# Kernel tuning notes

Measured on AMD Instinct MI355X. Metric: run time of the kernel, lower is better.

## Reference

```python
import jax, jax.numpy as jnp
import numpy as np

B, T, D, H = 8, 2048, 512, 128

def setup_inputs() -> dict:
    key = jax.random.key(0)
    ks = jax.random.split(key, 8)
    s = lambda fan_in: 1.0 / np.sqrt(fan_in)
    return {
        "x": jax.random.normal(ks[0], (B, T, D), jnp.float32),
        "prediction": jax.random.normal(ks[1], (B, T, D), jnp.float32),
        "Wq": jax.random.uniform(ks[2], (D, H), jnp.float32, -s(D), s(D)),
        "bq": jnp.zeros((H,), jnp.float32),
        "Wk": jax.random.uniform(ks[3], (D, H), jnp.float32, -s(D), s(D)),
        "bk": jnp.zeros((H,), jnp.float32),
        "Wv": jax.random.uniform(ks[4], (D, D), jnp.float32, -s(D), s(D)),
        "bv": jnp.zeros((D,), jnp.float32),
        "Wf": jax.random.uniform(ks[5], (2 * D, D), jnp.float32, -s(2 * D), s(2 * D)),
        "bf": jnp.zeros((D,), jnp.float32),
    }

def reference(x, prediction, Wq, bq, Wk, bk, Wv, bv, Wf, bf):
    # q,k: [B,T,H]; v: [B,T,D]
    q = jnp.einsum('btd,dh->bth', prediction, Wq) + bq
    k = jnp.einsum('btd,dh->bth', x, Wk) + bk
    v = jnp.einsum('btd,de->bte', x, Wv) + bv
    # unscaled attention scores [B,T,T]
    scores = jnp.einsum('bth,bsh->bts', q, k)
    attn = jax.nn.softmax(scores, axis=-1)
    attended = jnp.einsum('bts,bsd->btd', attn, v)
    fusion_input = jnp.concatenate([prediction, attended], axis=-1)  # [B,T,2D]
    return jax.nn.sigmoid(jnp.einsum('btf,fd->btd', fusion_input, Wf) + bf)
```

## Files before the change

### kernel.cpp

```cpp
#include <hip/hip_runtime.h>
#include <hip/hip_bf16.h>


#define APF_B 8
#define APF_T 2048
#define APF_D 512
#define APF_H 128
#define APF_M (APF_B * APF_T)

typedef unsigned short u16;
typedef __attribute__((ext_vector_type(8))) short short8;
typedef __attribute__((ext_vector_type(4))) float f32x4;

static __device__ __forceinline__ float bf2f(u16 u) {
    union { unsigned int i; float f; } w;
    w.i = ((unsigned int)u) << 16;
    return w.f;
}
static __device__ __forceinline__ u16 f2bf(float x) {
    union { float f; unsigned int u; } cv;
    cv.f = x;
    unsigned int u = cv.u + 0x7FFFu + ((cv.u >> 16) & 1u);
    return (u16)(u >> 16);
}

static __device__ __forceinline__ void load16_lds(const u16* g, u16* l) {
    __builtin_amdgcn_global_load_lds(
        (const __attribute__((address_space(1))) unsigned int*)g,
        (__attribute__((address_space(3))) unsigned int*)l,
        16, 0, 0);
}


__global__ __launch_bounds__(256) void cvt_pair(const float* __restrict__ in0,
                                                u16* __restrict__ out0,
                                                const float* __restrict__ in1,
                                                u16* __restrict__ out1, long n4)
{
    long i = blockIdx.x * 256L + threadIdx.x;
    const long stride = (long)gridDim.x * 256L;
    for (; i < 2 * n4; i += stride) {
        const float* in = (i < n4) ? in0 : in1;
        u16* out = (i < n4) ? out0 : out1;
        const long j = (i < n4) ? i : (i - n4);
        const float4 v = ((const float4*)in)[j];
        ushort4 o;
        o.x = f2bf(v.x); o.y = f2bf(v.y); o.z = f2bf(v.z); o.w = f2bf(v.w);
        ((ushort4*)out)[j] = o;
    }
}

__global__ __launch_bounds__(256) void prep_weights(
    const float* __restrict__ Wq, u16* __restrict__ WqT,
    const float* __restrict__ Wk, u16* __restrict__ WkT,
    const float* __restrict__ Wv, u16* __restrict__ WvT,
    const float* __restrict__ Wf, u16* __restrict__ WfT)
{
    const long e = blockIdx.x * 256L + threadIdx.x;
    if (e < 65536) {
        const long idx = e;
        const long n = idx / 512, k = idx % 512;
        WqT[idx] = f2bf(Wq[k * 128 + n]);
    } else if (e < 131072) {
        const long idx = e - 65536;
        const long n = idx / 512, k = idx % 512;
        WkT[idx] = f2bf(Wk[k * 128 + n]);
    } else if (e < 393216) {
        const long idx = e - 131072;
        const long n = idx / 512, k = idx % 512;
        WvT[idx] = f2bf(Wv[k * 512 + n]);
    } else if (e < 917504) {
        const long idx = e - 393216;
        const long n = idx / 1024, k = idx % 1024;
        WfT[idx] = f2bf(Wf[k * 512 + n]);
    }
}

template <int DUAL, int EPI>
__global__ __launch_bounds__(256) void mfma_gemm(
    const u16* __restrict__ Ap, const u16* __restrict__ A2p, long lda,
    const u16* __restrict__ Bp, const u16* __restrict__ Bp2, long ldb,
    const float* __restrict__ biasp, const float* __restrict__ bias2,
    void* __restrict__ Cp, void* __restrict__ Cp2, long ldc, int K,
    long sA, long sB, long sC)
{
    __shared__ u16 smA[128 * 32];
    __shared__ u16 smB[128 * 32];

    const int tid  = threadIdx.x;
    const int lane = tid & 63;
    const int wid  = tid >> 6;
    const int wr   = wid >> 1;
    const int wc   = wid & 1;

    const long row0 = (long)blockIdx.y * 128;
    const long col0 = (long)blockIdx.x * 128;
    const long z    = blockIdx.z;

    const u16* Abase = (DUAL == 2) ? (z ? A2p : Ap) : (Ap + z * sA);
    const u16* Bbase = (DUAL == 2) ? (z ? Bp2 : Bp) : (Bp + z * sB);

    f32x4 acc[4][4];
#pragma unroll
    for (int i = 0; i < 4; ++i)
#pragma unroll
        for (int j = 0; j < 4; ++j)
            acc[i][j] = (f32x4){0.f, 0.f, 0.f, 0.f};

    const int lrow = (lane >> 4) * 4;
    const int lcol = lane & 15;
    const int q8   = (lane >> 4) * 8;

    for (int kb = 0; kb < K; kb += 32) {
#pragma unroll
        for (int rep = 0; rep < 2; ++rep) {
            const int c  = tid + rep * 256;
            const int r  = c >> 2;
            const int kc = (c & 3) * 8;
            const int wbase = (wid * 64 + rep * 256) * 8;
            const u16* ga;
            if (DUAL == 1 && (kb + kc) >= APF_D) {
                ga = A2p + (row0 + r) * lda + (kb + kc - APF_D);
            } else {
                ga = Abase + (row0 + r) * lda + (kb + kc);
            }
            load16_lds(ga, &smA[wbase]);
            const u16* gb = Bbase + (col0 + r) * ldb + (kb + kc);
            load16_lds(gb, &smB[wbase]);
        }
        __syncthreads();

        short8 av[4], bv4[4];
#pragma unroll
        for (int ti = 0; ti < 4; ++ti)
            av[ti] = *(const short8*)&smA[(wr * 64 + ti * 16 + lcol) * 32 + q8];
#pragma unroll
        for (int tj = 0; tj < 4; ++tj)
            bv4[tj] = *(const short8*)&smB[(wc * 64 + tj * 16 + lcol) * 32 + q8];

#pragma unroll
        for (int ti = 0; ti < 4; ++ti)
#pragma unroll
            for (int tj = 0; tj < 4; ++tj)
                acc[ti][tj] = __builtin_amdgcn_mfma_f32_16x16x32_bf16(
                    av[ti], bv4[tj], acc[ti][tj], 0, 0, 0);
        __syncthreads();
    }

    const float* bias = (DUAL == 2 && z) ? bias2 : biasp;

#pragma unroll
    for (int ti = 0; ti < 4; ++ti) {
        const long m0t = row0 + wr * 64 + ti * 16 + lrow;
#pragma unroll
        for (int tj = 0; tj < 4; ++tj) {
            const long n = col0 + wc * 64 + tj * 16 + lcol;
            const float bn = (bias != nullptr) ? bias[n] : 0.f;
            if (EPI == 0) {
                u16* C = (u16*)((DUAL == 2 && z) ? Cp2 : Cp) + ((DUAL == 2) ? 0 : z * sC);
#pragma unroll
                for (int r = 0; r < 4; ++r)
                    C[(m0t + r) * ldc + n] = f2bf(acc[ti][tj][r] + bn);
            } else if (EPI == 1) {
                u16* C = (u16*)Cp;
                const long b  = m0t >> 11;
                const long ml = m0t & 2047;
                ushort4 pk;
                pk.x = f2bf(acc[ti][tj][0] + bn);
                pk.y = f2bf(acc[ti][tj][1] + bn);
                pk.z = f2bf(acc[ti][tj][2] + bn);
                pk.w = f2bf(acc[ti][tj][3] + bn);
                *(ushort4*)&C[b * (512L * 2048) + n * 2048 + ml] = pk;
            } else {
                float* C = (float*)Cp;
#pragma unroll
                for (int r = 0; r < 4; ++r) {
                    const float val = acc[ti][tj][r] + bn;
                    C[(m0t + r) * ldc + n] = 1.0f / (1.0f + expf(-val));
                }
            }
        }
    }
}

#define FA_LDQ 136
#define FA_LDK 136
#define FA_LDV 72
#define FA_LDP 72

__global__ __launch_bounds__(512, 2) void attn_fused(
    const u16* __restrict__ qg, const u16* __restrict__ kg,
    const u16* __restrict__ vTg, u16* __restrict__ attg)
{
    __shared__ u16 sQ[128 * FA_LDQ];
    __shared__ u16 sK[64 * FA_LDK];
    __shared__ u16 sV[256 * FA_LDV];
    __shared__ u16 sP[128 * FA_LDP];

    const int tid  = threadIdx.x;
    const int lane = tid & 63;
    const int w    = tid >> 6;
    const int l15  = lane & 15;
    const int q4   = lane >> 4;

    const long z  = blockIdx.z;
    const long q0 = (long)blockIdx.y * 128;
    const long d0 = (long)blockIdx.x * 256;

    {
        const u16* src = qg + (z * APF_T + q0) * APF_H;
#pragma unroll
        for (int rep = 0; rep < 4; ++rep) {
            const int c   = tid + rep * 512;
            const int row = c >> 4;
            const int c8  = (c & 15) * 8;
            *(uint4*)&sQ[row * FA_LDQ + c8] = *(const uint4*)(src + (long)c * 8);
        }
    }

    f32x4 oacc[16];
#pragma unroll
    for (int i = 0; i < 16; ++i) oacc[i] = (f32x4){0.f, 0.f, 0.f, 0.f};
    float rs[4] = {0.f, 0.f, 0.f, 0.f};

    for (int kt = 0; kt < APF_T / 64; ++kt) {
        __syncthreads();
        {
            const u16* src = kg + (z * APF_T + (long)kt * 64) * APF_H;
#pragma unroll
            for (int rep = 0; rep < 2; ++rep) {
                const int c   = tid + rep * 512;
                const int row = c >> 4;
                const int c8  = (c & 15) * 8;
                *(uint4*)&sK[row * FA_LDK + c8] = *(const uint4*)(src + (long)c * 8);
            }
        }
        {
            const u16* src = vTg + z * ((long)APF_D * APF_T) + d0 * APF_T + (long)kt * 64;
#pragma unroll
            for (int rep = 0; rep < 4; ++rep) {
                const int c   = tid + rep * 512;
                const int row = c >> 3;
                const int c8  = (c & 7) * 8;
                *(uint4*)&sV[row * FA_LDV + c8] =
                    *(const uint4*)(src + (long)row * APF_T + c8);
            }
        }
        __syncthreads();

        f32x4 sacc[4];
#pragma unroll
        for (int tj = 0; tj < 4; ++tj) sacc[tj] = (f32x4){0.f, 0.f, 0.f, 0.f};
#pragma unroll
        for (int kk = 0; kk < 4; ++kk) {
            const short8 av = *(const short8*)&sQ[(w * 16 + l15) * FA_LDQ + kk * 32 + q4 * 8];
#pragma unroll
            for (int tj = 0; tj < 4; ++tj) {
                const short8 bv = *(const short8*)&sK[(tj * 16 + l15) * FA_LDK + kk * 32 + q4 * 8];
                sacc[tj] = __builtin_amdgcn_mfma_f32_16x16x32_bf16(av, bv, sacc[tj], 0, 0, 0);
            }
        }
#pragma unroll
        for (int tj = 0; tj < 4; ++tj)
#pragma unroll
            for (int r = 0; r < 4; ++r) {
                const float e = __expf(sacc[tj][r]);
                rs[r] += e;
                sP[(w * 16 + q4 * 4 + r) * FA_LDP + tj * 16 + l15] = f2bf(e);
            }
#pragma unroll
        for (int kk = 0; kk < 2; ++kk) {
            const short8 ap = *(const short8*)&sP[(w * 16 + l15) * FA_LDP + kk * 32 + q4 * 8];
#pragma unroll
            for (int dt = 0; dt < 16; ++dt) {
                const short8 bv = *(const short8*)&sV[(dt * 16 + l15) * FA_LDV + kk * 32 + q4 * 8];
                oacc[dt] = __builtin_amdgcn_mfma_f32_16x16x32_bf16(ap, bv, oacc[dt], 0, 0, 0);
            }
        }
    }

#pragma unroll
    for (int r = 0; r < 4; ++r) {
        float s = rs[r];
        s += __shfl_xor(s, 1);
        s += __shfl_xor(s, 2);
        s += __shfl_xor(s, 4);
        s += __shfl_xor(s, 8);
        rs[r] = 1.0f / s;
    }

    const long mbase = z * APF_T + q0 + w * 16 + q4 * 4;
#pragma unroll
    for (int dt = 0; dt < 16; ++dt) {
        const long col = d0 + dt * 16 + l15;
#pragma unroll
        for (int r = 0; r < 4; ++r)
            attg[(mbase + r) * APF_D + col] = f2bf(oacc[dt][r] * rs[r]);
    }
}

extern "C" void kernel_launch(void* const* d_in, const int* in_sizes, int n_in,
                              void* d_out, int out_size, void* d_ws, size_t ws_size,
                              hipStream_t stream)
{
    (void)in_sizes; (void)n_in; (void)out_size; (void)ws_size;

    const float* x    = (const float*)d_in[0];
    const float* pred = (const float*)d_in[1];
    const float* Wq   = (const float*)d_in[2];
    const float* bq   = (const float*)d_in[3];
    const float* Wk   = (const float*)d_in[4];
    const float* bk   = (const float*)d_in[5];
    const float* Wv   = (const float*)d_in[6];
    const float* bv   = (const float*)d_in[7];
    const float* Wf   = (const float*)d_in[8];
    const float* bfu  = (const float*)d_in[9];

    u16* wsp   = (u16*)d_ws;
    u16* xb    = wsp;
    u16* predb = xb    + (long)APF_M * APF_D;
    u16* qb    = predb + (long)APF_M * APF_D;
    u16* kbuf  = qb    + (long)APF_M * APF_H;
    u16* vTb   = kbuf  + (long)APF_M * APF_H;
    u16* attb  = vTb   + (long)APF_M * APF_D;
    u16* WqT   = attb  + (long)APF_M * APF_D;
    u16* WkT   = WqT   + (long)APF_H * APF_D;
    u16* WvT   = WkT   + (long)APF_H * APF_D;
    u16* WfT   = WvT   + (long)APF_D * APF_D;

    const dim3 thr(256);
    const long nBTD4 = (long)APF_M * APF_D / 4;

    cvt_pair<<<dim3(1024), thr, 0, stream>>>(x, xb, pred, predb, nBTD4);
    prep_weights<<<dim3(3584), thr, 0, stream>>>(Wq, WqT, Wk, WkT, Wv, WvT, Wf, WfT);

    mfma_gemm<2, 0><<<dim3(1, 128, 2), thr, 0, stream>>>(
        predb, xb, APF_D, WqT, WkT, APF_D, bq, bk, qb, kbuf, APF_H, APF_D,
        0, 0, 0);

    mfma_gemm<0, 1><<<dim3(4, 128, 1), thr, 0, stream>>>(
        xb, nullptr, APF_D, WvT, nullptr, APF_D, bv, nullptr, vTb, nullptr,
        0, APF_D, 0, 0, 0);

    attn_fused<<<dim3(2, 16, 8), dim3(512), 0, stream>>>(qb, kbuf, vTb, attb);

    mfma_gemm<1, 2><<<dim3(4, 128, 1), thr, 0, stream>>>(
        predb, attb, APF_D, WfT, nullptr, 2 * APF_D, bfu, nullptr, d_out, nullptr,
        APF_D, 2 * APF_D, 0, 0, 0);
}
```

Measured before the change: 297.3 us.

## Halve attention query tile to 64 rows and compute V^T as batched transposed GEMM

```diff
diff --git a/kernel.cpp b/kernel.cpp
--- a/kernel.cpp
+++ b/kernel.cpp
@@ -76,7 +76,7 @@
     }
 }
 
-template <int DUAL, int EPI>
+template <int DUAL, int EPI, int BIASM>
 __global__ __launch_bounds__(256) void mfma_gemm(
     const u16* __restrict__ Ap, const u16* __restrict__ A2p, long lda,
     const u16* __restrict__ Bp, const u16* __restrict__ Bp2, long ldb,
@@ -155,22 +155,14 @@
 #pragma unroll
         for (int tj = 0; tj < 4; ++tj) {
             const long n = col0 + wc * 64 + tj * 16 + lcol;
-            const float bn = (bias != nullptr) ? bias[n] : 0.f;
+            const float bn = (BIASM == 0 && bias != nullptr) ? bias[n] : 0.f;
             if (EPI == 0) {
                 u16* C = (u16*)((DUAL == 2 && z) ? Cp2 : Cp) + ((DUAL == 2) ? 0 : z * sC);
 #pragma unroll
-                for (int r = 0; r < 4; ++r)
-                    C[(m0t + r) * ldc + n] = f2bf(acc[ti][tj][r] + bn);
-            } else if (EPI == 1) {
-                u16* C = (u16*)Cp;
-                const long b  = m0t >> 11;
-                const long ml = m0t & 2047;
-                ushort4 pk;
-                pk.x = f2bf(acc[ti][tj][0] + bn);
-                pk.y = f2bf(acc[ti][tj][1] + bn);
-                pk.z = f2bf(acc[ti][tj][2] + bn);
-                pk.w = f2bf(acc[ti][tj][3] + bn);
-                *(ushort4*)&C[b * (512L * 2048) + n * 2048 + ml] = pk;
+                for (int r = 0; r < 4; ++r) {
+                    const float bm = (BIASM == 1) ? bias[m0t + r] : bn;
+                    C[(m0t + r) * ldc + n] = f2bf(acc[ti][tj][r] + bm);
+                }
             } else {
                 float* C = (float*)Cp;
 #pragma unroll
@@ -188,14 +180,14 @@
 #define FA_LDV 72
 #define FA_LDP 72
 
-__global__ __launch_bounds__(512, 2) void attn_fused(
+__global__ __launch_bounds__(256, 2) void attn_fused(
     const u16* __restrict__ qg, const u16* __restrict__ kg,
     const u16* __restrict__ vTg, u16* __restrict__ attg)
 {
-    __shared__ u16 sQ[128 * FA_LDQ];
+    __shared__ u16 sQ[64 * FA_LDQ];
     __shared__ u16 sK[64 * FA_LDK];
     __shared__ u16 sV[256 * FA_LDV];
-    __shared__ u16 sP[128 * FA_LDP];
+    __shared__ u16 sP[64 * FA_LDP];
 
     const int tid  = threadIdx.x;
     const int lane = tid & 63;
@@ -204,14 +196,14 @@
     const int q4   = lane >> 4;
 
     const long z  = blockIdx.z;
-    const long q0 = (long)blockIdx.y * 128;
+    const long q0 = (long)blockIdx.y * 64;
     const long d0 = (long)blockIdx.x * 256;
 
     {
         const u16* src = qg + (z * APF_T + q0) * APF_H;
 #pragma unroll
         for (int rep = 0; rep < 4; ++rep) {
-            const int c   = tid + rep * 512;
+            const int c   = tid + rep * 256;
             const int row = c >> 4;
             const int c8  = (c & 15) * 8;
             *(uint4*)&sQ[row * FA_LDQ + c8] = *(const uint4*)(src + (long)c * 8);
@@ -228,8 +220,8 @@
         {
             const u16* src = kg + (z * APF_T + (long)kt * 64) * APF_H;
 #pragma unroll
-            for (int rep = 0; rep < 2; ++rep) {
-                const int c   = tid + rep * 512;
+            for (int rep = 0; rep < 4; ++rep) {
+                const int c   = tid + rep * 256;
                 const int row = c >> 4;
                 const int c8  = (c & 15) * 8;
                 *(uint4*)&sK[row * FA_LDK + c8] = *(const uint4*)(src + (long)c * 8);
@@ -238,8 +230,8 @@
         {
             const u16* src = vTg + z * ((long)APF_D * APF_T) + d0 * APF_T + (long)kt * 64;
 #pragma unroll
-            for (int rep = 0; rep < 4; ++rep) {
-                const int c   = tid + rep * 512;
+            for (int rep = 0; rep < 8; ++rep) {
+                const int c   = tid + rep * 256;
                 const int row = c >> 3;
                 const int c8  = (c & 7) * 8;
                 *(uint4*)&sV[row * FA_LDV + c8] =
@@ -334,17 +326,17 @@
     cvt_pair<<<dim3(1024), thr, 0, stream>>>(x, xb, pred, predb, nBTD4);
     prep_weights<<<dim3(3584), thr, 0, stream>>>(Wq, WqT, Wk, WkT, Wv, WvT, Wf, WfT);
 
-    mfma_gemm<2, 0><<<dim3(1, 128, 2), thr, 0, stream>>>(
+    mfma_gemm<2, 0, 0><<<dim3(1, 128, 2), thr, 0, stream>>>(
         predb, xb, APF_D, WqT, WkT, APF_D, bq, bk, qb, kbuf, APF_H, APF_D,
         0, 0, 0);
 
-    mfma_gemm<0, 1><<<dim3(4, 128, 1), thr, 0, stream>>>(
-        xb, nullptr, APF_D, WvT, nullptr, APF_D, bv, nullptr, vTb, nullptr,
-        0, APF_D, 0, 0, 0);
-
-    attn_fused<<<dim3(2, 16, 8), dim3(512), 0, stream>>>(qb, kbuf, vTb, attb);
-
-    mfma_gemm<1, 2><<<dim3(4, 128, 1), thr, 0, stream>>>(
+    mfma_gemm<0, 0, 1><<<dim3(16, 4, 8), thr, 0, stream>>>(
+        WvT, nullptr, APF_D, xb, nullptr, APF_D, bv, nullptr, vTb, nullptr,
+        APF_T, APF_D, 0, (long)APF_T * APF_D, (long)APF_D * APF_T);
+
+    attn_fused<<<dim3(2, 32, 8), thr, 0, stream>>>(qb, kbuf, vTb, attb);
+
+    mfma_gemm<1, 2, 0><<<dim3(4, 128, 1), thr, 0, stream>>>(
         predb, attb, APF_D, WfT, nullptr, 2 * APF_D, bfu, nullptr, d_out, nullptr,
         APF_D, 2 * APF_D, 0, 0, 0);
 }
```

After: 291.0 us. 2.1% less time.
